# Performance work log

Hardware: AMD Instinct MI355X
Metric: run time of the kernel (lower is better)

The kernel has to match this reference:

```python
import jax, jax.numpy as jnp
import numpy as np

NEG = jnp.float32(-1e30)  # finite stand-in for -inf (keeps grads NaN-free)

B, S = 8, 256


def _inside_logZ(scores, mask):
    """CYK inside algorithm. scores/mask: [B, S, S]. Returns scalar logZ.

    Recurrence (widths w = 1..S-1, processed as a scan over anti-diagonals):
      s[i, i+1] = scores[i, i+1]
      s[i, i+w] = scores[i, i+w] + logsumexp_{k=i+1..i+w-1} (s[i, k] + s[k, i+w])
    logZ = sum_b s[b, 0, lens[b]].
    """
    Bsz, Sl, _ = scores.shape
    lens = mask[:, 0].sum(-1)                    # [B] sentence lengths
    idx = jnp.arange(Sl)
    rows = idx[:, None]                          # [S,1] span start i
    m = idx[None, :]                             # [1,S] split offset (k = i+m)
    km = jnp.clip(rows + m, 0, Sl - 1)           # [S,S] split index k, clipped reads

    def step(s, w):
        # s: [B,S,S] chart. Process all spans of width w at once.
        j = jnp.clip(rows + w, 0, Sl - 1)        # [S,1] span end (clipped)
        left = s[:, rows, km]                    # s[b, i, i+m]      -> [B,S,S]
        right = s[:, km, j]                      # s[b, i+m, i+w]    -> [B,S,S]
        valid = (m >= 1) & (m <= w - 1) & (rows + w < Sl)
        lse = jax.nn.logsumexp(jnp.where(valid, left + right, NEG), axis=-1)  # [B,S]
        diag = scores[:, idx, jnp.clip(idx + w, 0, Sl - 1)]                    # [B,S]
        val = diag + jnp.where(w == 1, 0.0, lse)
        # scatter onto the w-th diagonal; out-of-range (i+w >= S) lanes dropped
        s = s.at[:, idx, idx + w].set(val, mode='drop')
        return s, None

    s0 = jnp.full((Bsz, Sl, Sl), NEG, scores.dtype)
    s, _ = jax.lax.scan(step, s0, jnp.arange(1, Sl))
    return s[jnp.arange(Bsz), 0, lens].sum()


def setup_inputs() -> dict:
    key = jax.random.key(0)
    scores = jax.random.normal(key, (B, S, S), dtype=jnp.float32)
    # strict upper-triangular mask (all sentences full length S-1 tokens)
    mask = jnp.triu(jnp.ones((S, S), dtype=bool), k=1)
    mask = jnp.broadcast_to(mask, (B, S, S))
    return {"scores": scores, "mask": mask}


def reference(scores, mask):
    # forward(scores, mask, target=None, mbr=True): marginals = d logZ / d scores
    marginals = jax.grad(lambda sc: _inside_logZ(sc, mask))(scores)
    return marginals
```

## Files before the change

### kernel.cpp

```cpp
#include <hip/hip_runtime.h>

#define SL 256
#define BATCH 8
#define NT 1024
#define W0 16
#define LDSF 33152
#define TABN 264
#define LDSB ((LDSF + 32 + TABN + 256) * 4)

__device__ __forceinline__ int rowOff(int j) {
  int jp = (j > 128) ? (256 - j) : j;
  int base = (jp - 1) * 260;
  if (j > 128) base += (jp + 3) & ~3;
  return base;
}

template <int G>
__device__ __forceinline__ float grpSum(float v) {
#pragma unroll
  for (int o = G >> 1; o; o >>= 1) v += __shfl_xor(v, o, 64);
  return v;
}

__device__ __forceinline__ void barrier_lgkm() {
  __builtin_amdgcn_sched_barrier(0);
  asm volatile("s_waitcnt lgkmcnt(0)" ::: "memory");
  __builtin_amdgcn_s_barrier();
  __builtin_amdgcn_sched_barrier(0);
}

__device__ void rescaleE(int tid, float dc, int wcur, float* sh, float* E1,
                         const int* __restrict__ tab) {
  const int lane = tid & 63, wave = tid >> 6;
  for (int j = 1 + wave; j < SL; j += 16) {
    int jlo = j - wcur; if (jlo < 0) jlo = 0;
    int base = tab[j];
    for (int i = jlo + lane; i < j; i += 64)
      sh[base + i] *= __expf(-dc * (float)(j - i));
  }
  const float f1 = __expf(-dc);
  for (int i = tid; i < SL - 1; i += NT) E1[i] *= f1;
}

template <int G>
__device__ void insideP(int wlo, int whi, int tid, const float* __restrict__ sc,
                        float* __restrict__ sh, float* __restrict__ red,
                        const int* __restrict__ tab, float* __restrict__ E1) {
  constexpr int LG = (G == 4) ? 2 : (G == 8) ? 3 : (G == 16) ? 4 : 5;
  constexpr int NG = 64 / G;
  const int lane = tid & 63, wv = tid >> 6;
  const int l = lane >> LG, lig = lane & (G - 1);
  const int i = wv * (NG - 1) + l;
  for (int w = wlo; w <= whi; w += 2) {
    const int t = ((w - 17) >> 1) + 1;
    const float fl = red[16 + ((t - 1) & 1)];
    const unsigned wm1 = (unsigned)(w - 1);
    const unsigned wm2 = (unsigned)(w - 2);
    const bool vw = i < SL - w;
    const bool vw1 = (l < NG - 1) && (i < SL - w - 1);
    const int jw = (i + w < SL) ? i + w : SL - 1;
    const int jw1 = (i + w + 1 < SL) ? i + w + 1 : SL - 1;
    const int ojw = tab[jw], ojw1 = tab[jw1];
    const float scw = sc[i * SL + jw];
    const float scw1 = sc[i * SL + jw1];
    float a0 = 0.f, a1 = 0.f, b0 = 0.f, b1 = 0.f;
    if (vw) {
      for (int s4 = ((i + 1) & ~3) + 4 * lig; s4 < i + w; s4 += 4 * G) {
        float4 rw = *(const float4*)(sh + ojw + s4);
        float4 rw1 = *(const float4*)(sh + ojw1 + s4);
        int4 tv = *(const int4*)(tab + s4);
        float e0 = sh[tv.x + i], e1 = sh[tv.y + i];
        float e2 = sh[tv.z + i], e3 = sh[tv.w + i];
        const int d0 = s4 - i;
        float f0 = ((unsigned)(d0 - 1) < wm1) ? e0 : 0.f;
        float f1 = ((unsigned)(d0    ) < wm1) ? e1 : 0.f;
        float f2 = ((unsigned)(d0 + 1) < wm1) ? e2 : 0.f;
        float f3 = ((unsigned)(d0 + 2) < wm1) ? e3 : 0.f;
        a0 = fmaf(f0, rw.x, a0); a1 = fmaf(f1, rw.y, a1);
        a0 = fmaf(f2, rw.z, a0); a1 = fmaf(f3, rw.w, a1);
        float g0 = ((unsigned)(d0 - 2) < wm2) ? e0 : 0.f;
        float g1 = ((unsigned)(d0 - 1) < wm2) ? e1 : 0.f;
        float g2 = ((unsigned)(d0    ) < wm2) ? e2 : 0.f;
        float g3 = ((unsigned)(d0 + 1) < wm2) ? e3 : 0.f;
        b0 = fmaf(g0, rw1.x, b0); b1 = fmaf(g1, rw1.y, b1);
        b0 = fmaf(g2, rw1.z, b0); b1 = fmaf(g3, rw1.w, b1);
      }
    }
    float accw = grpSum<G>(a0 + a1);
    float accw1 = grpSum<G>(b0 + b1);
    float Ew = __expf(scw) * accw;
    if (vw && lig == 0) {
      sh[ojw + i] = Ew;
      if (accw > 3.5e19f || accw < 3e-16f) red[16 + (t & 1)] = fmaxf(accw, 1e-30f);
    }
    float EwN = __shfl_down(Ew, G, 64);
    if (vw1) {
      float tot = accw1 + E1[i] * EwN + Ew * E1[jw];
      if (lig == 0) {
        sh[ojw1 + i] = __expf(scw1) * tot;
        if (tot > 3.5e19f || tot < 3e-16f) red[16 + (t & 1)] = fmaxf(tot, 1e-30f);
      }
    }
    __syncthreads();
    if (fl != 0.f) {
      float dc = (__logf(fl) + 8.0f) / (float)(w - 2);
      rescaleE(tid, dc, w + 1, sh, E1, tab);
      __syncthreads();
      if (tid == 0) { red[16] = 0.f; red[17] = 0.f; }
      __syncthreads();
    }
  }
}

template <int G>
__device__ void outsideP(int wAhi, int wAlo, int tid, const float* __restrict__ sc,
                         float* __restrict__ gOut, const float* __restrict__ Eg,
                         const float* __restrict__ ETg, float* __restrict__ shH,
                         const int* __restrict__ tab, const float* __restrict__ E1) {
  constexpr int LG = (G == 4) ? 2 : (G == 8) ? 3 : (G == 16) ? 4 : 5;
  constexpr int NG = 64 / G;
  const int lane = tid & 63, wv = tid >> 6;
  const int l = lane >> LG, lig = lane & (G - 1);
  const int p = wv * (NG - 1) + l;
  for (int wA = wAhi; wA >= wAlo; wA -= 2) {
    const int wB = wA - 1;
    const bool vA = p < SL - wA;
    const bool vB = (l >= 1 || wv == 0) && (p < SL - wB);
    const int qA = p + wA, qB = p + wB;
    const int qAc = (qA < SL) ? qA : SL - 1;
    const int qBc = (qB < SL) ? qB : SL - 1;
    const int oA = tab[qAc], oB = tab[qBc];
    const float scA = sc[p * SL + qAc];
    const float scB = sc[p * SL + qBc];
    float EpA = 0.f, EpB = 0.f;
    if (lig == 0) {
      if (vA) EpA = Eg[p * SL + qA];
      if (vB) EpB = Eg[p * SL + qB];
    }
    float a0 = 0.f, a1 = 0.f, b0 = 0.f, b1 = 0.f;
    if (vA || vB) {
      const float* erA = Eg + (size_t)qAc * SL;
      const float* erB = Eg + (size_t)qBc * SL;
      for (int s4 = ((qA + 1) & ~3) + 4 * lig; s4 < SL; s4 += 4 * G) {
        float4 eA = *(const float4*)(erA + s4);
        float4 eB = *(const float4*)(erB + s4);
        int4 tv = *(const int4*)(tab + s4);
        float h0 = shH[tv.x + p], h1 = shH[tv.y + p];
        float h2 = shH[tv.z + p], h3 = shH[tv.w + p];
        float m0 = (s4 + 0 > qA) ? h0 : 0.f, m1 = (s4 + 1 > qA) ? h1 : 0.f;
        float m2 = (s4 + 2 > qA) ? h2 : 0.f, m3 = (s4 + 3 > qA) ? h3 : 0.f;
        a0 = fmaf(eA.x, m0, a0); a1 = fmaf(eA.y, m1, a1);
        a0 = fmaf(eA.z, m2, a0); a1 = fmaf(eA.w, m3, a1);
        b0 = fmaf(eB.x, m0, b0); b1 = fmaf(eB.y, m1, b1);
        b0 = fmaf(eB.z, m2, b0); b1 = fmaf(eB.w, m3, b1);
      }
      for (int s4 = 4 * lig; s4 < p; s4 += 4 * G) {
        float4 ev = *(const float4*)(ETg + (size_t)p * SL + s4);
        float4 hA = *(const float4*)(shH + oA + s4);
        float4 hB = *(const float4*)(shH + oB + s4);
        a0 = fmaf(ev.x, hA.x, a0); a1 = fmaf(ev.y, hA.y, a1);
        a0 = fmaf(ev.z, hA.z, a0); a1 = fmaf(ev.w, hA.w, a1);
        float n0 = (s4 + 0 < p - 1) ? hB.x : 0.f;
        float n1 = (s4 + 1 < p - 1) ? hB.y : 0.f;
        float n2 = (s4 + 2 < p - 1) ? hB.z : 0.f;
        float n3 = (s4 + 3 < p - 1) ? hB.w : 0.f;
        b0 = fmaf(ev.x, n0, b0); b1 = fmaf(ev.y, n1, b1);
        b0 = fmaf(ev.z, n2, b0); b1 = fmaf(ev.w, n3, b1);
      }
    }
    float accA = grpSum<G>(a0 + a1);
    float accBb = grpSum<G>(b0 + b1);
    float HA = __expf(scA) * accA;
    if (vA && lig == 0) {
      shH[oA + p] = HA;
      gOut[p * SL + qA] = EpA * accA;
    }
    float HAup = __shfl_up(HA, G, 64);
    if (vB) {
      float accB = accBb + (vA ? E1[qB] * HA : 0.f)
                         + ((p > 0) ? E1[p - 1] * HAup : 0.f);
      if (lig == 0) {
        shH[oB + p] = __expf(scB) * accB;
        gOut[p * SL + qB] = EpB * accB;
      }
    }
    barrier_lgkm();
  }
}

template <int G>
__device__ void outsideB(int w0, int w1, int tid,
    const float* __restrict__ sc, float* __restrict__ gOut,
    const float* __restrict__ Eg, const float* __restrict__ ETg,
    float* __restrict__ shH, const int* __restrict__ tab) {
  constexpr int LG = (G == 4) ? 2 : (G == 8) ? 3 : (G == 16) ? 4 : (G == 32) ? 5 : 6;
  const int c = tid >> LG, lig = tid & (G - 1);
  for (int w = w0; w >= w1; --w) {
    if (c < SL - w) {
      const int p = c, q = p + w;
      float scv = 0.f, Epq = 0.f;
      if (lig == 0) { scv = sc[p * SL + q]; Epq = Eg[p * SL + q]; }
      float a0 = 0.f, a1 = 0.f;
      const float* er = Eg + (size_t)q * SL;
      for (int s4 = ((q + 1) & ~3) + 4 * lig; s4 < SL; s4 += 4 * G) {
        float4 ev = *(const float4*)(er + s4);
        int4 tv = *(const int4*)(tab + s4);
        float h0 = shH[tv.x + p], h1 = shH[tv.y + p];
        float h2 = shH[tv.z + p], h3 = shH[tv.w + p];
        a0 = fmaf(ev.x, (s4 + 0 > q) ? h0 : 0.f, a0);
        a1 = fmaf(ev.y, (s4 + 1 > q) ? h1 : 0.f, a1);
        a0 = fmaf(ev.z, (s4 + 2 > q) ? h2 : 0.f, a0);
        a1 = fmaf(ev.w, (s4 + 3 > q) ? h3 : 0.f, a1);
      }
      if (p > 0) {
        const float* et = ETg + (size_t)p * SL;
        const float* hq = shH + tab[q];
        for (int s4 = 4 * lig; s4 < p; s4 += 4 * G) {
          float4 ev = *(const float4*)(et + s4);
          float4 hv = *(const float4*)(hq + s4);
          a0 = fmaf(ev.x, hv.x, a0);
          a1 = fmaf(ev.y, hv.y, a1);
          a0 = fmaf(ev.z, hv.z, a0);
          a1 = fmaf(ev.w, hv.w, a1);
        }
      }
      float acc = grpSum<G>(a0 + a1);
      if (lig == 0) {
        gOut[p * SL + q] = Epq * acc;
        shH[tab[q] + p] = acc * __expf(scv);
      }
    }
    barrier_lgkm();
  }
}

__global__ __launch_bounds__(NT) void cyk_pair(
    const float* __restrict__ scores, float* __restrict__ out,
    float* __restrict__ ws) {
  extern __shared__ float sh[];
  float* red = sh + LDSF;
  int* tab = (int*)(sh + LDSF + 32);
  float* E1 = sh + LDSF + 32 + TABN;
  const int b = blockIdx.x;
  const int tid = threadIdx.x;
  const int lane = tid & 63;
  const int wave = tid >> 6;
  const size_t P = (size_t)SL * SL;
  const float* sc = scores + (size_t)b * P;
  float* g   = out + (size_t)b * P;
  float* Eg  = ws + (size_t)b * P;
  float* ETg = ws + (size_t)(BATCH + b) * P;

  for (int idx = tid * 4; idx < LDSF; idx += NT * 4)
    *(float4*)(sh + idx) = make_float4(0.f, 0.f, 0.f, 0.f);
  if (tid < 32) red[tid] = 0.f;
  if (tid < TABN) tab[tid] = (tid >= 1 && tid <= 255) ? rowOff(tid) : 0;
  __syncthreads();

  for (int i = tid; i < SL - 1; i += NT)
    sh[tab[i + 1] + i] = sc[i * SL + i + 1];
  __syncthreads();

  {
    const int c4 = tid >> 2, lig = tid & 3;
    for (int w = 2; w <= W0; ++w) {
      if (c4 < SL - w) {
        const int i = c4, j = i + w;
        const int oj = tab[j];
        float scv = 0.f;
        if (lig == 0) scv = sc[i * SL + j];
        float m = -1e30f, sum = 0.f;
        for (int k = i + 1 + lig; k < j; k += 4) {
          float t = sh[tab[k] + i] + sh[oj + k];
          float nm = fmaxf(m, t);
          sum = sum * __expf(m - nm) + __expf(t - nm);
          m = nm;
        }
#pragma unroll
        for (int o = 2; o; o >>= 1) {
          float mo = __shfl_xor(m, o, 64);
          float so = __shfl_xor(sum, o, 64);
          float nm = fmaxf(m, mo);
          sum = sum * __expf(m - nm) + so * __expf(mo - nm);
          m = nm;
        }
        if (lig == 0) sh[oj + i] = scv + m + __logf(sum);
      }
      __syncthreads();
    }
  }

  {
    int idx = tid < SL - W0 ? tid : SL - W0 - 1;
    float v = sh[tab[idx + W0] + idx];
#pragma unroll
    for (int o = 32; o; o >>= 1) v = fmaxf(v, __shfl_xor(v, o, 64));
    if (lane == 0) red[wave] = v;
  }
  __syncthreads();
  float cc;
  {
    float mx = red[0];
#pragma unroll
    for (int t = 1; t < 16; ++t) mx = fmaxf(mx, red[t]);
    cc = mx / (float)W0;
  }

  for (int w = 1; w <= W0; ++w) {
    for (int i = tid; i < SL - w; i += NT) {
      int o = tab[i + w] + i;
      float E = __expf(sh[o] - cc * (float)w);
      sh[o] = E;
      if (w == 1) E1[i] = E;
    }
  }
  if (tid == 0) { red[16] = 0.f; red[17] = 0.f; }
  __syncthreads();

  insideP<4>(17, 141, tid, sc, sh, red, tab, E1);
  insideP<8>(143, 205, tid, sc, sh, red, tab, E1);
  insideP<16>(207, 237, tid, sc, sh, red, tab, E1);
  insideP<32>(239, 253, tid, sc, sh, red, tab, E1);

  {
    float acc = 0.f;
    if (wave == 0) {
      const int o255 = tab[255];
      for (int k = 1 + lane; k < 255; k += 64)
        acc += sh[tab[k]] * sh[o255 + k];
#pragma unroll
      for (int o = 32; o; o >>= 1) acc += __shfl_xor(acc, o, 64);
      if (lane == 0) sh[o255] = __expf(sc[SL - 1]) * acc;
    }
    __syncthreads();
  }

  for (int idx = tid; idx < SL * SL; idx += NT) {
    int j = idx >> 8, i = idx & 255;
    if (i < j) ETg[idx] = sh[tab[j] + i];
  }
  for (int idx = tid; idx < SL * SL; idx += NT) {
    int i = idx >> 8, k = idx & 255;
    if (k > i) Eg[idx] = sh[tab[k] + i];
  }
  if (tid == 0) {
    float Er = sh[tab[SL - 1]];
    red[20] = (Er > 0.f) ? __expf(sc[SL - 1]) / Er : 0.f;
    g[SL - 1] = 1.0f;
  }
  __syncthreads();

  for (int idx = tid * 4; idx < LDSF; idx += NT * 4)
    *(float4*)(sh + idx) = make_float4(0.f, 0.f, 0.f, 0.f);
  __syncthreads();
  if (tid == 0) sh[tab[SL - 1]] = red[20];
  __syncthreads();

  outsideP<32>(254, 240, tid, sc, g, Eg, ETg, sh, tab, E1);
  outsideP<16>(238, 208, tid, sc, g, Eg, ETg, sh, tab, E1);
  outsideP<8>(206, 144, tid, sc, g, Eg, ETg, sh, tab, E1);
  outsideP<4>(142, 16, tid, sc, g, Eg, ETg, sh, tab, E1);
  outsideB<4>(14, 1, tid, sc, g, Eg, ETg, sh, tab);
}

__device__ __forceinline__ float grpMaxR(float v, int G) {
#pragma unroll
  for (int o = 32; o; o >>= 1)
    if (o < G) v = fmaxf(v, __shfl_xor(v, o, 64));
  return v;
}
__device__ __forceinline__ float grpSumR(float v, int G) {
#pragma unroll
  for (int o = 32; o; o >>= 1)
    if (o < G) v += __shfl_xor(v, o, 64);
  return v;
}

__global__ __launch_bounds__(NT) void cyk_io_fb(
    const float* __restrict__ scores, float* __restrict__ out,
    float* __restrict__ ws) {
  const int b = blockIdx.x;
  const int tid = threadIdx.x;
  const size_t P = (size_t)SL * SL;
  const float* sc = scores + (size_t)b * P;
  float* g = out + (size_t)b * P;
  float* s = ws + (size_t)b * P;
  float* l = ws + (size_t)(BATCH + b) * P;

  for (int i = tid; i < SL - 1; i += NT) {
    s[i * SL + i + 1] = sc[i * SL + i + 1];
    l[i * SL + i + 1] = 0.f;
  }
  __syncthreads();

  for (int w = 2; w < SL; ++w) {
    const int cells = SL - w;
    int G = NT / cells;
    G = (G >= 64) ? 64 : (1 << (31 - __clz(G)));
    const int lg = 31 - __clz(G);
    const int c = tid >> lg;
    const int lig = tid & (G - 1);
    if (c < cells) {
      const int i = c, j = i + w;
      const float* srow = s + i * SL;
      float m = -INFINITY;
      for (int k = i + 1 + lig; k < j; k += G)
        m = fmaxf(m, srow[k] + s[k * SL + j]);
      m = grpMaxR(m, G);
      float sum = 0.f;
      for (int k = i + 1 + lig; k < j; k += G)
        sum += __expf(srow[k] + s[k * SL + j] - m);
      sum = grpSumR(sum, G);
      if (lig == 0) {
        const float lse = m + __logf(sum);
        s[i * SL + j] = sc[i * SL + j] + lse;
        l[i * SL + j] = lse;
      }
    }
    __syncthreads();
  }

  if (tid == 0) g[0 * SL + (SL - 1)] = 1.0f;
  __syncthreads();

  for (int w = SL - 2; w >= 1; --w) {
    const int cells = SL - w;
    int G = NT / cells;
    G = (G >= 64) ? 64 : (1 << (31 - __clz(G)));
    const int lg = 31 - __clz(G);
    const int c = tid >> lg;
    const int lig = tid & (G - 1);
    if (c < cells) {
      const int p = c, q = p + w;
      const float spq = s[p * SL + q];
      const int TR = SL - 1 - q;
      const int T = TR + p;
      float acc = 0.f;
      for (int t = lig; t < T; t += G) {
        if (t < TR) {
          const int j = q + 1 + t;
          acc += g[p * SL + j] * __expf(spq + s[q * SL + j] - l[p * SL + j]);
        } else {
          const int i = t - TR;
          acc += g[i * SL + q] * __expf(s[i * SL + p] + spq - l[i * SL + q]);
        }
      }
      acc = grpSumR(acc, G);
      if (lig == 0) g[p * SL + q] = acc;
    }
    __syncthreads();
  }
}

extern "C" void kernel_launch(void* const* d_in, const int* in_sizes, int n_in,
                              void* d_out, int out_size, void* d_ws, size_t ws_size,
                              hipStream_t stream) {
  const float* scores = (const float*)d_in[0];
  float* out = (float*)d_out;
  float* ws = (float*)d_ws;

  const size_t sq = (size_t)SL * SL * sizeof(float);
  hipMemsetAsync(d_out, 0, (size_t)BATCH * sq, stream);

  int dev = 0;
  hipGetDevice(&dev);
  int maxShm = 0;
  hipDeviceGetAttribute(&maxShm, hipDeviceAttributeMaxSharedMemoryPerBlock, dev);
  (void)hipFuncSetAttribute(reinterpret_cast<const void*>(cyk_pair),
                            hipFuncAttributeMaxDynamicSharedMemorySize, LDSB);

  if (maxShm >= LDSB && ws_size >= (size_t)2 * BATCH * sq) {
    hipMemsetAsync(ws, 0, (size_t)2 * BATCH * sq, stream);
    cyk_pair<<<BATCH, NT, LDSB, stream>>>(scores, out, ws);
  } else {
    cyk_io_fb<<<BATCH, NT, 0, stream>>>(scores, out, ws);
  }
}
```

Before: 703.8 us.

## Process four CYK diagonals per barrier in inside and outside passes

Extends the paired-diagonal scheme to quads: each iteration computes widths w..w+3 together, doing the dependent short-split terms in registers via shuffles and stored width-1/2/3 span values (Es1..Es3). This removes about half of the block-wide barriers in both the sequential inside and outside sweeps. In exchange it uses more registers and extra LDS for the Es arrays, and each group covers fewer valid spans (NG-3 per wave), so work per span can be less balanced.

```diff
diff --git a/kernel.cpp b/kernel.cpp
--- a/kernel.cpp
+++ b/kernel.cpp
@@ -6,7 +6,7 @@
 #define W0 16
 #define LDSF 33152
 #define TABN 264
-#define LDSB ((LDSF + 32 + TABN + 256) * 4)
+#define LDSB ((LDSF + 32 + TABN + 3 * 256) * 4)
 
 __device__ __forceinline__ int rowOff(int j) {
   int jp = (j > 128) ? (256 - j) : j;
@@ -29,7 +29,8 @@
   __builtin_amdgcn_sched_barrier(0);
 }
 
-__device__ void rescaleE(int tid, float dc, int wcur, float* sh, float* E1,
+__device__ void rescaleE(int tid, float dc, int wcur, float* sh,
+                         float* Es1, float* Es2, float* Es3,
                          const int* __restrict__ tab) {
   const int lane = tid & 63, wave = tid >> 6;
   for (int j = 1 + wave; j < SL; j += 16) {
@@ -39,20 +40,26 @@
       sh[base + i] *= __expf(-dc * (float)(j - i));
   }
   const float f1 = __expf(-dc);
-  for (int i = tid; i < SL - 1; i += NT) E1[i] *= f1;
+  const float f2 = f1 * f1;
+  const float f3 = f2 * f1;
+  for (int x = tid; x < SL; x += NT) {
+    Es1[x] *= f1; Es2[x] *= f2; Es3[x] *= f3;
+  }
 }
 
 template <int G>
-__device__ void insideP(int wlo, int whi, int tid, const float* __restrict__ sc,
-                        float* __restrict__ sh, float* __restrict__ red,
-                        const int* __restrict__ tab, float* __restrict__ E1) {
+__device__ void insideP(int wlo, int whi, int t0, int tid,
+                        const float* __restrict__ sc, float* __restrict__ sh,
+                        float* __restrict__ red, const int* __restrict__ tab,
+                        float* __restrict__ Es1, float* __restrict__ Es2,
+                        float* __restrict__ Es3) {
   constexpr int LG = (G == 4) ? 2 : (G == 8) ? 3 : (G == 16) ? 4 : 5;
   constexpr int NG = 64 / G;
   const int lane = tid & 63, wv = tid >> 6;
   const int l = lane >> LG, lig = lane & (G - 1);
   const int i = wv * (NG - 1) + l;
   for (int w = wlo; w <= whi; w += 2) {
-    const int t = ((w - 17) >> 1) + 1;
+    const int t = t0 + ((w - wlo) >> 1);
     const float fl = red[16 + ((t - 1) & 1)];
     const unsigned wm1 = (unsigned)(w - 1);
     const unsigned wm2 = (unsigned)(w - 2);
@@ -95,7 +102,7 @@
     }
     float EwN = __shfl_down(Ew, G, 64);
     if (vw1) {
-      float tot = accw1 + E1[i] * EwN + Ew * E1[jw];
+      float tot = accw1 + Es1[i] * EwN + Ew * Es1[jw];
       if (lig == 0) {
         sh[ojw1 + i] = __expf(scw1) * tot;
         if (tot > 3.5e19f || tot < 3e-16f) red[16 + (t & 1)] = fmaxf(tot, 1e-30f);
@@ -104,7 +111,113 @@
     __syncthreads();
     if (fl != 0.f) {
       float dc = (__logf(fl) + 8.0f) / (float)(w - 2);
-      rescaleE(tid, dc, w + 1, sh, E1, tab);
+      rescaleE(tid, dc, w + 1, sh, Es1, Es2, Es3, tab);
+      __syncthreads();
+      if (tid == 0) { red[16] = 0.f; red[17] = 0.f; }
+      __syncthreads();
+    }
+  }
+}
+
+template <int G>
+__device__ void insideQ(int wlo, int whi, int t0, int tid,
+                        const float* __restrict__ sc, float* __restrict__ sh,
+                        float* __restrict__ red, const int* __restrict__ tab,
+                        float* __restrict__ Es1, float* __restrict__ Es2,
+                        float* __restrict__ Es3) {
+  constexpr int LG = (G == 4) ? 2 : 3;
+  constexpr int NG = 64 / G;
+  const int lane = tid & 63, wv = tid >> 6;
+  const int l = lane >> LG, lig = lane & (G - 1);
+  const int i = wv * (NG - 3) + l;
+  for (int w = wlo; w <= whi; w += 4) {
+    const int t = t0 + ((w - wlo) >> 2);
+    const float fl = red[16 + ((t - 1) & 1)];
+    const bool v0 = i < SL - w;
+    const bool v1 = i < SL - w - 1;
+    const bool v2 = i < SL - w - 2;
+    const bool v3 = i < SL - w - 3;
+    const int j0 = (i + w < SL) ? i + w : SL - 1;
+    const int j1 = (i + w + 1 < SL) ? i + w + 1 : SL - 1;
+    const int j2 = (i + w + 2 < SL) ? i + w + 2 : SL - 1;
+    const int j3 = (i + w + 3 < SL) ? i + w + 3 : SL - 1;
+    const int o0 = tab[j0], o1 = tab[j1], o2 = tab[j2], o3 = tab[j3];
+    const int rb = i * SL;
+    const float s0 = sc[rb + j0], s1 = sc[rb + j1];
+    const float s2 = sc[rb + j2], s3 = sc[rb + j3];
+    float a0=0.f,a1=0.f,b0=0.f,b1=0.f,c0=0.f,c1=0.f,e4a=0.f,e4b=0.f;
+    if (v0) {
+      const unsigned mA = (unsigned)(w - 1);
+      const unsigned mB = (unsigned)(w - 2);
+      const unsigned mC = (unsigned)(w - 3);
+      const unsigned mD = (unsigned)(w - 4);
+      for (int s4 = ((i + 1) & ~3) + 4 * lig; s4 < i + w; s4 += 4 * G) {
+        float4 r0 = *(const float4*)(sh + o0 + s4);
+        float4 r1 = *(const float4*)(sh + o1 + s4);
+        float4 r2 = *(const float4*)(sh + o2 + s4);
+        float4 r3 = *(const float4*)(sh + o3 + s4);
+        int4 tv = *(const int4*)(tab + s4);
+        float e0 = sh[tv.x + i], e1 = sh[tv.y + i];
+        float e2 = sh[tv.z + i], e3 = sh[tv.w + i];
+        const int dd = s4 - i;
+        float f0 = ((unsigned)(dd - 1) < mA) ? e0 : 0.f;
+        float f1 = ((unsigned)(dd    ) < mA) ? e1 : 0.f;
+        float f2 = ((unsigned)(dd + 1) < mA) ? e2 : 0.f;
+        float f3 = ((unsigned)(dd + 2) < mA) ? e3 : 0.f;
+        a0 = fmaf(f0, r0.x, a0); a1 = fmaf(f1, r0.y, a1);
+        a0 = fmaf(f2, r0.z, a0); a1 = fmaf(f3, r0.w, a1);
+        float g0 = ((unsigned)(dd - 2) < mB) ? e0 : 0.f;
+        float g1 = ((unsigned)(dd - 1) < mB) ? e1 : 0.f;
+        float g2 = ((unsigned)(dd    ) < mB) ? e2 : 0.f;
+        float g3 = ((unsigned)(dd + 1) < mB) ? e3 : 0.f;
+        b0 = fmaf(g0, r1.x, b0); b1 = fmaf(g1, r1.y, b1);
+        b0 = fmaf(g2, r1.z, b0); b1 = fmaf(g3, r1.w, b1);
+        float h0 = ((unsigned)(dd - 3) < mC) ? e0 : 0.f;
+        float h1 = ((unsigned)(dd - 2) < mC) ? e1 : 0.f;
+        float h2 = ((unsigned)(dd - 1) < mC) ? e2 : 0.f;
+        float h3 = ((unsigned)(dd    ) < mC) ? e3 : 0.f;
+        c0 = fmaf(h0, r2.x, c0); c1 = fmaf(h1, r2.y, c1);
+        c0 = fmaf(h2, r2.z, c0); c1 = fmaf(h3, r2.w, c1);
+        float k0 = ((unsigned)(dd - 4) < mD) ? e0 : 0.f;
+        float k1 = ((unsigned)(dd - 3) < mD) ? e1 : 0.f;
+        float k2 = ((unsigned)(dd - 2) < mD) ? e2 : 0.f;
+        float k3 = ((unsigned)(dd - 1) < mD) ? e3 : 0.f;
+        e4a = fmaf(k0, r3.x, e4a); e4b = fmaf(k1, r3.y, e4b);
+        e4a = fmaf(k2, r3.z, e4a); e4b = fmaf(k3, r3.w, e4b);
+      }
+    }
+    float A0 = grpSum<G>(a0 + a1);
+    float A1 = grpSum<G>(b0 + b1);
+    float A2 = grpSum<G>(c0 + c1);
+    float A3 = grpSum<G>(e4a + e4b);
+    const float es1i = Es1[i], es2i = Es2[i], es3i = Es3[i];
+    const float E0 = __expf(s0) * A0;
+    const float n10 = __shfl_down(E0, G, 64);
+    const float n20 = __shfl_down(E0, 2 * G, 64);
+    const float n30 = __shfl_down(E0, 3 * G, 64);
+    const float T1 = A1 + es1i * n10 + E0 * Es1[j0];
+    const float E1v = __expf(s1) * T1;
+    const float n11 = __shfl_down(E1v, G, 64);
+    const float n21 = __shfl_down(E1v, 2 * G, 64);
+    const float T2 = A2 + es1i * n11 + E1v * Es1[j1] + es2i * n20 + E0 * Es2[j0];
+    const float E2v = __expf(s2) * T2;
+    const float n12 = __shfl_down(E2v, G, 64);
+    const float T3 = A3 + es1i * n12 + E2v * Es1[j2] + es2i * n21 + E1v * Es2[j1]
+                        + es3i * n30 + E0 * Es3[j0];
+    const float E3v = __expf(s3) * T3;
+    if (lig == 0) {
+      if (v0)                sh[o0 + i] = E0;
+      if (v1 && l <= NG - 2) sh[o1 + i] = E1v;
+      if (v2 && l <= NG - 3) sh[o2 + i] = E2v;
+      if (v3 && l <= NG - 4) sh[o3 + i] = E3v;
+      if (v0 && (A0 > 3.5e19f || A0 < 3e-16f)) red[16 + (t & 1)] = fmaxf(A0, 1e-30f);
+      if (v3 && l <= NG - 4 && (T3 > 3.5e19f || T3 < 3e-16f))
+        red[16 + (t & 1)] = fmaxf(T3, 1e-30f);
+    }
+    __syncthreads();
+    if (fl != 0.f) {
+      float dc = (__logf(fl) + 8.0f) / (float)(w - 3);
+      rescaleE(tid, dc, w + 3, sh, Es1, Es2, Es3, tab);
       __syncthreads();
       if (tid == 0) { red[16] = 0.f; red[17] = 0.f; }
       __syncthreads();
@@ -116,7 +229,7 @@
 __device__ void outsideP(int wAhi, int wAlo, int tid, const float* __restrict__ sc,
                          float* __restrict__ gOut, const float* __restrict__ Eg,
                          const float* __restrict__ ETg, float* __restrict__ shH,
-                         const int* __restrict__ tab, const float* __restrict__ E1) {
+                         const int* __restrict__ tab, const float* __restrict__ Es1) {
   constexpr int LG = (G == 4) ? 2 : (G == 8) ? 3 : (G == 16) ? 4 : 5;
   constexpr int NG = 64 / G;
   const int lane = tid & 63, wv = tid >> 6;
@@ -177,12 +290,133 @@
     }
     float HAup = __shfl_up(HA, G, 64);
     if (vB) {
-      float accB = accBb + (vA ? E1[qB] * HA : 0.f)
-                         + ((p > 0) ? E1[p - 1] * HAup : 0.f);
+      float accB = accBb + (vA ? Es1[qBc] * HA : 0.f)
+                         + ((p > 0) ? Es1[p - 1] * HAup : 0.f);
       if (lig == 0) {
         shH[oB + p] = __expf(scB) * accB;
         gOut[p * SL + qB] = EpB * accB;
       }
+    }
+    barrier_lgkm();
+  }
+}
+
+template <int G>
+__device__ void outsideQ(int wAhi, int wAlo, int tid, const float* __restrict__ sc,
+                         float* __restrict__ gOut, const float* __restrict__ Eg,
+                         const float* __restrict__ ETg, float* __restrict__ shH,
+                         const int* __restrict__ tab, const float* __restrict__ Es1,
+                         const float* __restrict__ Es2, const float* __restrict__ Es3) {
+  constexpr int LG = (G == 4) ? 2 : 3;
+  constexpr int NG = 64 / G;
+  const int lane = tid & 63, wv = tid >> 6;
+  const int l = lane >> LG, lig = lane & (G - 1);
+  const int p = wv * (NG - 3) + l;
+  for (int wA = wAhi; wA >= wAlo; wA -= 4) {
+    const bool v0 = p < SL - wA;
+    const bool v1 = p < SL - wA + 1;
+    const bool v2 = p < SL - wA + 2;
+    const bool v3 = p < SL - wA + 3;
+    const int q0 = p + wA, q1 = q0 - 1, q2 = q0 - 2, q3 = q0 - 3;
+    const int qc0 = (q0 < SL) ? q0 : SL - 1;
+    const int qc1 = (q1 < SL) ? q1 : SL - 1;
+    const int qc2 = (q2 < SL) ? q2 : SL - 1;
+    const int qc3 = (q3 < SL) ? q3 : SL - 1;
+    const int o0 = tab[qc0], o1 = tab[qc1], o2 = tab[qc2], o3 = tab[qc3];
+    const int rb = p * SL;
+    const float s0 = sc[rb + qc0], s1 = sc[rb + qc1];
+    const float s2 = sc[rb + qc2], s3 = sc[rb + qc3];
+    float Ep0 = 0.f, Ep1 = 0.f, Ep2 = 0.f, Ep3 = 0.f;
+    if (lig == 0) {
+      if (v0) Ep0 = Eg[rb + q0];
+      if (v1) Ep1 = Eg[rb + q1];
+      if (v2) Ep2 = Eg[rb + q2];
+      if (v3) Ep3 = Eg[rb + q3];
+    }
+    float a0=0.f,a1=0.f,b0=0.f,b1=0.f,c0=0.f,c1=0.f,e4a=0.f,e4b=0.f;
+    if (v3) {
+      const float* er0 = Eg + (size_t)qc0 * SL;
+      const float* er1 = Eg + (size_t)qc1 * SL;
+      const float* er2 = Eg + (size_t)qc2 * SL;
+      const float* er3 = Eg + (size_t)qc3 * SL;
+      for (int s4 = ((q0 + 1) & ~3) + 4 * lig; s4 < SL; s4 += 4 * G) {
+        float4 e0v = *(const float4*)(er0 + s4);
+        float4 e1v = *(const float4*)(er1 + s4);
+        float4 e2v = *(const float4*)(er2 + s4);
+        float4 e3v = *(const float4*)(er3 + s4);
+        int4 tv = *(const int4*)(tab + s4);
+        float h0 = (s4 + 0 > q0) ? shH[tv.x + p] : 0.f;
+        float h1 = (s4 + 1 > q0) ? shH[tv.y + p] : 0.f;
+        float h2 = (s4 + 2 > q0) ? shH[tv.z + p] : 0.f;
+        float h3 = (s4 + 3 > q0) ? shH[tv.w + p] : 0.f;
+        a0 = fmaf(e0v.x, h0, a0); a1 = fmaf(e0v.y, h1, a1);
+        a0 = fmaf(e0v.z, h2, a0); a1 = fmaf(e0v.w, h3, a1);
+        b0 = fmaf(e1v.x, h0, b0); b1 = fmaf(e1v.y, h1, b1);
+        b0 = fmaf(e1v.z, h2, b0); b1 = fmaf(e1v.w, h3, b1);
+        c0 = fmaf(e2v.x, h0, c0); c1 = fmaf(e2v.y, h1, c1);
+        c0 = fmaf(e2v.z, h2, c0); c1 = fmaf(e2v.w, h3, c1);
+        e4a = fmaf(e3v.x, h0, e4a); e4b = fmaf(e3v.y, h1, e4b);
+        e4a = fmaf(e3v.z, h2, e4a); e4b = fmaf(e3v.w, h3, e4b);
+      }
+      for (int s4 = 4 * lig; s4 < p; s4 += 4 * G) {
+        float4 ev = *(const float4*)(ETg + (size_t)p * SL + s4);
+        float4 h0v = *(const float4*)(shH + o0 + s4);
+        float4 h1v = *(const float4*)(shH + o1 + s4);
+        float4 h2v = *(const float4*)(shH + o2 + s4);
+        float4 h3v = *(const float4*)(shH + o3 + s4);
+        a0 = fmaf(ev.x, h0v.x, a0); a1 = fmaf(ev.y, h0v.y, a1);
+        a0 = fmaf(ev.z, h0v.z, a0); a1 = fmaf(ev.w, h0v.w, a1);
+        float n0 = (s4 + 0 < p - 1) ? h1v.x : 0.f;
+        float n1 = (s4 + 1 < p - 1) ? h1v.y : 0.f;
+        float n2 = (s4 + 2 < p - 1) ? h1v.z : 0.f;
+        float n3 = (s4 + 3 < p - 1) ? h1v.w : 0.f;
+        b0 = fmaf(ev.x, n0, b0); b1 = fmaf(ev.y, n1, b1);
+        b0 = fmaf(ev.z, n2, b0); b1 = fmaf(ev.w, n3, b1);
+        float x0 = (s4 + 0 < p - 2) ? h2v.x : 0.f;
+        float x1 = (s4 + 1 < p - 2) ? h2v.y : 0.f;
+        float x2 = (s4 + 2 < p - 2) ? h2v.z : 0.f;
+        float x3 = (s4 + 3 < p - 2) ? h2v.w : 0.f;
+        c0 = fmaf(ev.x, x0, c0); c1 = fmaf(ev.y, x1, c1);
+        c0 = fmaf(ev.z, x2, c0); c1 = fmaf(ev.w, x3, c1);
+        float y0 = (s4 + 0 < p - 3) ? h3v.x : 0.f;
+        float y1 = (s4 + 1 < p - 3) ? h3v.y : 0.f;
+        float y2 = (s4 + 2 < p - 3) ? h3v.z : 0.f;
+        float y3 = (s4 + 3 < p - 3) ? h3v.w : 0.f;
+        e4a = fmaf(ev.x, y0, e4a); e4b = fmaf(ev.y, y1, e4b);
+        e4a = fmaf(ev.z, y2, e4a); e4b = fmaf(ev.w, y3, e4b);
+      }
+    }
+    float A0 = grpSum<G>(a0 + a1);
+    float A1 = grpSum<G>(b0 + b1);
+    float A2 = grpSum<G>(c0 + c1);
+    float A3 = grpSum<G>(e4a + e4b);
+    const float ep1 = (p >= 1) ? Es1[p - 1] : 0.f;
+    const float ep2 = (p >= 2) ? Es2[p - 2] : 0.f;
+    const float ep3 = (p >= 3) ? Es3[p - 3] : 0.f;
+    const float H0 = __expf(s0) * A0;
+    const float u10 = __shfl_up(H0, G, 64);
+    const float u20 = __shfl_up(H0, 2 * G, 64);
+    const float u30 = __shfl_up(H0, 3 * G, 64);
+    const float T1 = A1 + (v0 ? Es1[qc1] * H0 : 0.f) + ep1 * u10;
+    const float H1 = __expf(s1) * T1;
+    const float u11 = __shfl_up(H1, G, 64);
+    const float u21 = __shfl_up(H1, 2 * G, 64);
+    const float T2 = A2 + (v1 ? Es1[qc2] * H1 : 0.f) + ep1 * u11
+                        + (v0 ? Es2[qc2] * H0 : 0.f) + ep2 * u20;
+    const float H2 = __expf(s2) * T2;
+    const float u12 = __shfl_up(H2, G, 64);
+    const float T3 = A3 + (v2 ? Es1[qc3] * H2 : 0.f) + ep1 * u12
+                        + (v1 ? Es2[qc3] * H1 : 0.f) + ep2 * u21
+                        + (v0 ? Es3[qc3] * H0 : 0.f) + ep3 * u30;
+    const float H3 = __expf(s3) * T3;
+    const bool okl1 = (l >= 1) || (wv == 0);
+    const bool okl2 = (l >= 2) || (wv == 0);
+    const bool okl3 = (l >= 3) || (wv == 0);
+    if (lig == 0) {
+      if (v0)         { shH[o0 + p] = H0; gOut[rb + q0] = Ep0 * A0; }
+      if (v1 && okl1) { shH[o1 + p] = H1; gOut[rb + q1] = Ep1 * T1; }
+      if (v2 && okl2) { shH[o2 + p] = H2; gOut[rb + q2] = Ep2 * T2; }
+      if (v3 && okl3) { shH[o3 + p] = H3; gOut[rb + q3] = Ep3 * T3; }
     }
     barrier_lgkm();
   }
@@ -234,13 +468,15 @@
   }
 }
 
-__global__ __launch_bounds__(NT) void cyk_pair(
+__global__ __launch_bounds__(NT) void cyk_quad(
     const float* __restrict__ scores, float* __restrict__ out,
     float* __restrict__ ws) {
   extern __shared__ float sh[];
   float* red = sh + LDSF;
   int* tab = (int*)(sh + LDSF + 32);
-  float* E1 = sh + LDSF + 32 + TABN;
+  float* Es1 = sh + LDSF + 32 + TABN;
+  float* Es2 = Es1 + 256;
+  float* Es3 = Es2 + 256;
   const int b = blockIdx.x;
   const int tid = threadIdx.x;
   const int lane = tid & 63;
@@ -255,6 +491,7 @@
     *(float4*)(sh + idx) = make_float4(0.f, 0.f, 0.f, 0.f);
   if (tid < 32) red[tid] = 0.f;
   if (tid < TABN) tab[tid] = (tid >= 1 && tid <= 255) ? rowOff(tid) : 0;
+  if (tid < 256) { Es1[tid] = 0.f; Es2[tid] = 0.f; Es3[tid] = 0.f; }
   __syncthreads();
 
   for (int i = tid; i < SL - 1; i += NT)
@@ -311,16 +548,18 @@
       int o = tab[i + w] + i;
       float E = __expf(sh[o] - cc * (float)w);
       sh[o] = E;
-      if (w == 1) E1[i] = E;
+      if (w == 1) Es1[i] = E;
+      if (w == 2) Es2[i] = E;
+      if (w == 3) Es3[i] = E;
     }
   }
   if (tid == 0) { red[16] = 0.f; red[17] = 0.f; }
   __syncthreads();
 
-  insideP<4>(17, 141, tid, sc, sh, red, tab, E1);
-  insideP<8>(143, 205, tid, sc, sh, red, tab, E1);
-  insideP<16>(207, 237, tid, sc, sh, red, tab, E1);
-  insideP<32>(239, 253, tid, sc, sh, red, tab, E1);
+  insideP<4>(17, 43, 1, tid, sc, sh, red, tab, Es1, Es2, Es3);
+  insideQ<4>(45, 169, 15, tid, sc, sh, red, tab, Es1, Es2, Es3);
+  insideQ<8>(173, 249, 47, tid, sc, sh, red, tab, Es1, Es2, Es3);
+  insideP<32>(253, 253, 67, tid, sc, sh, red, tab, Es1, Es2, Es3);
 
   {
     float acc = 0.f;
@@ -356,11 +595,11 @@
   if (tid == 0) sh[tab[SL - 1]] = red[20];
   __syncthreads();
 
-  outsideP<32>(254, 240, tid, sc, g, Eg, ETg, sh, tab, E1);
-  outsideP<16>(238, 208, tid, sc, g, Eg, ETg, sh, tab, E1);
-  outsideP<8>(206, 144, tid, sc, g, Eg, ETg, sh, tab, E1);
-  outsideP<4>(142, 16, tid, sc, g, Eg, ETg, sh, tab, E1);
-  outsideB<4>(14, 1, tid, sc, g, Eg, ETg, sh, tab);
+  outsideP<32>(254, 254, tid, sc, g, Eg, ETg, sh, tab, Es1);
+  outsideQ<8>(252, 176, tid, sc, g, Eg, ETg, sh, tab, Es1, Es2, Es3);
+  outsideQ<4>(172, 48, tid, sc, g, Eg, ETg, sh, tab, Es1, Es2, Es3);
+  outsideP<4>(44, 18, tid, sc, g, Eg, ETg, sh, tab, Es1);
+  outsideB<4>(16, 1, tid, sc, g, Eg, ETg, sh, tab);
 }
 
 __device__ __forceinline__ float grpMaxR(float v, int G) {
@@ -466,12 +705,12 @@
   hipGetDevice(&dev);
   int maxShm = 0;
   hipDeviceGetAttribute(&maxShm, hipDeviceAttributeMaxSharedMemoryPerBlock, dev);
-  (void)hipFuncSetAttribute(reinterpret_cast<const void*>(cyk_pair),
+  (void)hipFuncSetAttribute(reinterpret_cast<const void*>(cyk_quad),
                             hipFuncAttributeMaxDynamicSharedMemorySize, LDSB);
 
   if (maxShm >= LDSB && ws_size >= (size_t)2 * BATCH * sq) {
     hipMemsetAsync(ws, 0, (size_t)2 * BATCH * sq, stream);
-    cyk_pair<<<BATCH, NT, LDSB, stream>>>(scores, out, ws);
+    cyk_quad<<<BATCH, NT, LDSB, stream>>>(scores, out, ws);
   } else {
     cyk_io_fb<<<BATCH, NT, 0, stream>>>(scores, out, ws);
   }
```

Measured after the change: 653.7 us. 7.1% less time.
